# Optimization experiments

Measured on AMD Instinct MI355X. Metric: run time of the kernel, lower is better.

The kernel has to match this reference:

```python
import jax, jax.numpy as jnp
import numpy as np

B, C_IN, C_OUT = 2, 32, 32
N_IN = 128 * 128            # input grid points
N_OUT = 128 * 128           # output grid points
KERNEL_SIZE = 9             # (3-1)*4 + 1 for kernel_shape=[3,4], piecewise_linear basis
NNZ = 1_500_000             # sparse entries in psi (kernel_size, n_out, n_in)


def setup_inputs() -> dict:
    key = jax.random.key(0)
    ks = jax.random.split(key, 8)
    scale = (1.0 / C_IN) ** 0.5  # sqrt(1/groupsize), groups=1
    return {
        "x": jax.random.normal(ks[0], (B, C_IN, N_IN), jnp.float32),
        "quadrature_weights": jax.random.uniform(ks[1], (N_IN,), jnp.float32, 0.5, 1.5) / N_IN,
        "psi_vals": jax.random.uniform(ks[2], (NNZ,), jnp.float32),
        "weight": scale * jax.random.normal(ks[3], (C_OUT, C_IN, KERNEL_SIZE), jnp.float32),
        "bias": jnp.zeros((C_OUT,), jnp.float32),
        "psi_idx_k": jax.random.randint(ks[4], (NNZ,), 0, KERNEL_SIZE, dtype=jnp.int32),
        "psi_idx_out": jax.random.randint(ks[5], (NNZ,), 0, N_OUT, dtype=jnp.int32),
        "psi_idx_in": jax.random.randint(ks[6], (NNZ,), 0, N_IN, dtype=jnp.int32),
        "n_out": N_OUT,
    }


def reference(x, quadrature_weights, psi_vals, weight, bias,
              psi_idx_k, psi_idx_out, psi_idx_in, n_out):
    # x: (B, C, n_in); weight: (O, C, K); psi is sparse (K, n_out, n_in)
    Bb, C, n_in = x.shape
    K = weight.shape[2]
    # pre-multiply by quadrature weights, layout (n_in, B, C) for gather
    xq = (x * quadrature_weights[None, None, :]).transpose(2, 0, 1)
    # gather-weight: contribution of each sparse entry  -> (nnz, B, C)
    contrib = xq[psi_idx_in] * psi_vals[:, None, None]
    # scatter-add into (kernel, out) bins == sparse psi @ xq
    seg = psi_idx_k * n_out + psi_idx_out
    xk = jax.ops.segment_sum(contrib, seg, num_segments=K * n_out)
    xk = xk.reshape(K, n_out, Bb, C)  # (K, n_out, B, C)
    # channel/kernel mixing with learned weight (groups=1)
    out = jnp.einsum("knbc,ock->bon", xk, weight) + bias[None, :, None]
    return out  # (B, out_channels, n_out)
```

## Files before the change

kernel.cpp:

```cpp
#include <hip/hip_runtime.h>

#define N_IN   16384
#define N_OUT  16384
#define KSZ    9
#define CIN    32
#define COUT   32
#define BC     64
#define NCB    256
#define CHA    4096
#define ECAP_A 8192
#define ROWS   144
#define XSTR   68
#define SCAP   2048

union PrepSH {
    struct { int cnt[NCB]; int cntE[NCB]; int gbase[NCB]; int cursor[NCB];
             float2 slist[CHA]; } bin;
    struct { float tile[64 * 65]; } xqp;
};

__global__ __launch_bounds__(512) void k_prep(
        const float* __restrict__ x, const float* __restrict__ qw,
        const float* __restrict__ vals, const float* __restrict__ w,
        const int* __restrict__ ik, const int* __restrict__ io,
        const int* __restrict__ ii, float* __restrict__ xq,
        float2* __restrict__ sivA, int* __restrict__ gcntA,
        float* __restrict__ wT, int nnz, int nchA) {
    __shared__ PrepSH sh;
    const int t = threadIdx.x;
    const int bid = blockIdx.x;

    if (bid >= nchA) {
        if (bid < nchA + 256) {
            const int in0 = (bid - nchA) * 64;
#pragma unroll
            for (int i = 0; i < 8; ++i) {
                int idx = t + i * 512;
                int bcl = idx >> 6, inl = idx & 63;
                sh.xqp.tile[bcl * 65 + inl] = x[bcl * N_IN + in0 + inl];
            }
            __syncthreads();
#pragma unroll
            for (int i = 0; i < 8; ++i) {
                int idx = t + i * 512;
                int inl = idx >> 6, bcl = idx & 63;
                xq[(size_t)(in0 + inl) * BC + bcl] = sh.xqp.tile[bcl * 65 + inl] * qw[in0 + inl];
            }
        } else {
            for (int i = t; i < COUT * CIN * KSZ; i += 512) {
                int o = i / (CIN * KSZ);
                int r = i - o * (CIN * KSZ);
                int c = r / KSZ;
                int k = r - c * KSZ;
                wT[((k * 8 + (o >> 2)) * 32 + c) * 4 + (o & 3)] = w[i];
            }
        }
        return;
    }

    if (t < NCB) sh.bin.cnt[t] = 0;
    __syncthreads();
    const int base = bid * CHA;
    const int e0   = base + t * 8;

    float vv[8]; int pk[8]; int bk[8]; bool hv[8];
    if (e0 + 8 <= nnz) {
        int4 a0 = *(const int4*)(io + e0),  a1 = *(const int4*)(io + e0 + 4);
        int4 b0 = *(const int4*)(ii + e0),  b1 = *(const int4*)(ii + e0 + 4);
        int4 k0 = *(const int4*)(ik + e0),  k1 = *(const int4*)(ik + e0 + 4);
        float4 d0 = *(const float4*)(vals + e0), d1 = *(const float4*)(vals + e0 + 4);
        int ov[8] = {a0.x, a0.y, a0.z, a0.w, a1.x, a1.y, a1.z, a1.w};
        int iv[8] = {b0.x, b0.y, b0.z, b0.w, b1.x, b1.y, b1.z, b1.w};
        int kv[8] = {k0.x, k0.y, k0.z, k0.w, k1.x, k1.y, k1.z, k1.w};
        float dv[8] = {d0.x, d0.y, d0.z, d0.w, d1.x, d1.y, d1.z, d1.w};
#pragma unroll
        for (int j = 0; j < 8; ++j) {
            hv[j] = true;
            bk[j] = ov[j] >> 6;
            pk[j] = (int)(((unsigned)(ov[j] >> 4) << 22)) | (iv[j] << 8) | (kv[j] * 16 + (ov[j] & 15));
            vv[j] = dv[j];
        }
    } else {
#pragma unroll
        for (int j = 0; j < 8; ++j) {
            int e = e0 + j;
            hv[j] = (e < nnz);
            if (hv[j]) {
                int o = io[e];
                bk[j] = o >> 6;
                pk[j] = (int)(((unsigned)(o >> 4) << 22)) | (ii[e] << 8) | (ik[e] * 16 + (o & 15));
                vv[j] = vals[e];
            } else { bk[j] = 0; pk[j] = 0; vv[j] = 0.f; }
        }
    }
#pragma unroll
    for (int j = 0; j < 8; ++j) if (hv[j]) atomicAdd(&sh.bin.cnt[bk[j]], 1);
    __syncthreads();
    if (t < NCB) {
        int cv = sh.bin.cnt[t];
        sh.bin.gbase[t] = t * ECAP_A + (cv ? atomicAdd(&gcntA[t], cv) : 0);
    }
    if (t < 64) {
        int carry = 0;
#pragma unroll
        for (int seg = 0; seg < 4; ++seg) {
            int idx = seg * 64 + t;
            int v = sh.bin.cnt[idx];
            int orig = v;
#pragma unroll
            for (int off = 1; off < 64; off <<= 1) {
                int u = __shfl_up(v, off);
                if (t >= off) v += u;
            }
            sh.bin.cntE[idx]   = carry + v - orig;
            sh.bin.cursor[idx] = carry + v - orig;
            carry += __shfl(v, 63);
        }
    }
    __syncthreads();
#pragma unroll
    for (int j = 0; j < 8; ++j) {
        if (hv[j]) {
            int pos = atomicAdd(&sh.bin.cursor[bk[j]], 1);
            sh.bin.slist[pos] = make_float2(vv[j], __int_as_float(pk[j]));
        }
    }
    __syncthreads();
    const int m = min(nnz - base, CHA);
    for (int p = t; p < m; p += 512) {
        float2 f2 = sh.bin.slist[p];
        int cb = (int)((unsigned)__float_as_int(f2.y) >> 24);
        int dest = sh.bin.gbase[cb] + (p - sh.bin.cntE[cb]);
        if (dest < (cb + 1) * ECAP_A) sivA[dest] = f2;
    }
}

__global__ __launch_bounds__(512) void k_fused6(const float* __restrict__ xq,
        const float2* __restrict__ sivA, const int* __restrict__ gcntA,
        const float* __restrict__ wT, const float* __restrict__ bias,
        float* __restrict__ out) {
    __shared__ __align__(16) float sxk[80 * XSTR];
    __shared__ float2 slist[SCAP];
    __shared__ int    rowStart[ROWS + 1];
    __shared__ int    cursor[ROWS];
    __shared__ int    mcur;
    const int tid  = threadIdx.x;
    const int lane = tid & 63;
    const int wv   = __builtin_amdgcn_readfirstlane(tid >> 6);
    const unsigned f = ((blockIdx.x & 7) << 7) | (blockIdx.x >> 3);

    if (tid < ROWS) rowStart[tid] = 0;
    if (tid == 0) mcur = 0;
    __syncthreads();

    const int cb = (int)(f >> 2);
    const int mA = min(gcntA[cb], ECAP_A);
    const float2* src = sivA + (size_t)cb * ECAP_A;
    float2* tmp = (float2*)sxk;
    for (int i = tid; i < mA; i += 512) {
        float2 v = src[i];
        unsigned fid = (unsigned)__float_as_int(v.y) >> 22;
        if (fid == f) {
            int pos = atomicAdd(&mcur, 1);
            if (pos < SCAP) {
                tmp[pos] = v;
                atomicAdd(&rowStart[__float_as_int(v.y) & 0xFF], 1);
            }
        }
    }
    __syncthreads();
    const int m2 = min(mcur, SCAP);
    if (wv == 0) {
        int carry = 0;
#pragma unroll
        for (int i0 = 0; i0 < 192; i0 += 64) {
            int idx = i0 + lane;
            int v = (idx < ROWS) ? rowStart[idx] : 0;
            int orig = v;
#pragma unroll
            for (int off = 1; off < 64; off <<= 1) {
                int u = __shfl_up(v, off);
                if (lane >= off) v += u;
            }
            if (idx < ROWS) {
                int excl = carry + v - orig;
                rowStart[idx] = excl;
                cursor[idx]   = excl;
            }
            carry += __shfl(v, 63);
        }
        if (lane == 0) rowStart[ROWS] = carry;
    }
    __syncthreads();
    for (int i = tid; i < m2; i += 512) {
        float2 v = tmp[i];
        int p = __float_as_int(v.y);
        int pos = atomicAdd(&cursor[p & 0xFF], 1);
        slist[pos] = make_float2(v.x, __int_as_float(p & 0x3FFF00));
    }
    __syncthreads();

    const char* xqb   = (const char*)xq;
    const int   lane4 = lane * 4;
    const int   h     = lane >> 4;
    const int   nl    = lane & 15;
    float acc[4] = {0.f, 0.f, 0.f, 0.f};

#pragma unroll
    for (int ph = 0; ph < 2; ++ph) {
        const int rbase = ph ? 80 : 0;
        const int rend  = ph ? 144 : 80;
        const int nrows = rend - rbase;
        for (int i = tid; i < nrows * XSTR; i += 512) sxk[i] = 0.f;
        __syncthreads();
        for (int r = rbase + wv; r < rend; r += 8) {
            const int a = rowStart[r], b = rowStart[r + 1];
            if (a >= b) continue;
            float acc0 = 0.f, acc1 = 0.f, acc2 = 0.f, acc3 = 0.f;
            int i = a;
            for (; i + 7 < b; i += 8) {
                float2 v0 = slist[i],     v1 = slist[i + 1], v2 = slist[i + 2], v3 = slist[i + 3];
                float2 v4 = slist[i + 4], v5 = slist[i + 5], v6 = slist[i + 6], v7 = slist[i + 7];
                acc0 += *(const float*)(xqb + (__float_as_int(v0.y) + lane4)) * v0.x;
                acc1 += *(const float*)(xqb + (__float_as_int(v1.y) + lane4)) * v1.x;
                acc2 += *(const float*)(xqb + (__float_as_int(v2.y) + lane4)) * v2.x;
                acc3 += *(const float*)(xqb + (__float_as_int(v3.y) + lane4)) * v3.x;
                acc0 += *(const float*)(xqb + (__float_as_int(v4.y) + lane4)) * v4.x;
                acc1 += *(const float*)(xqb + (__float_as_int(v5.y) + lane4)) * v5.x;
                acc2 += *(const float*)(xqb + (__float_as_int(v6.y) + lane4)) * v6.x;
                acc3 += *(const float*)(xqb + (__float_as_int(v7.y) + lane4)) * v7.x;
            }
            for (; i + 3 < b; i += 4) {
                float2 v0 = slist[i], v1 = slist[i + 1], v2 = slist[i + 2], v3 = slist[i + 3];
                acc0 += *(const float*)(xqb + (__float_as_int(v0.y) + lane4)) * v0.x;
                acc1 += *(const float*)(xqb + (__float_as_int(v1.y) + lane4)) * v1.x;
                acc2 += *(const float*)(xqb + (__float_as_int(v2.y) + lane4)) * v2.x;
                acc3 += *(const float*)(xqb + (__float_as_int(v3.y) + lane4)) * v3.x;
            }
            for (; i < b; ++i) {
                float2 v = slist[i];
                acc0 += *(const float*)(xqb + (__float_as_int(v.y) + lane4)) * v.x;
            }
            sxk[(r - rbase) * XSTR + lane] = (acc0 + acc1) + (acc2 + acc3);
        }
        __syncthreads();
        if (lane < 32) {
            const int kbase = ph ? 5 : 0;
            const int kcnt  = ph ? 4 : 5;
            for (int kk = 0; kk < kcnt; ++kk) {
                const float* xr = &sxk[(kk * 16 + nl) * XSTR + h * 32];
                const float* wp = &wT[((kbase + kk) * 8 + wv) * 128];
#pragma unroll
                for (int c4 = 0; c4 < 8; ++c4) {
                    float4 xv = *(const float4*)&xr[c4 * 4];
#pragma unroll
                    for (int cc = 0; cc < 4; ++cc) {
                        float xval = (&xv.x)[cc];
#pragma unroll
                        for (int j = 0; j < 4; ++j)
                            acc[j] += xval * wp[(c4 * 4 + cc) * 4 + j];
                    }
                }
            }
        }
        __syncthreads();
    }

    if (lane < 32) {
        const int n0 = (int)f * 16;
#pragma unroll
        for (int j = 0; j < 4; ++j) {
            int o = wv * 4 + j;
            out[((size_t)h * COUT + o) * N_OUT + n0 + nl] = acc[j] + bias[o];
        }
    }
}

extern "C" void kernel_launch(void* const* d_in, const int* in_sizes, int n_in,
                              void* d_out, int out_size, void* d_ws, size_t ws_size,
                              hipStream_t stream) {
    const float* x    = (const float*)d_in[0];
    const float* qw   = (const float*)d_in[1];
    const float* vals = (const float*)d_in[2];
    const float* w    = (const float*)d_in[3];
    const float* bias = (const float*)d_in[4];
    const int*   ik   = (const int*)d_in[5];
    const int*   io   = (const int*)d_in[6];
    const int*   ii   = (const int*)d_in[7];
    const int    nnz  = in_sizes[2];
    const int    nchA = (nnz + CHA - 1) / CHA;

    char* ws = (char*)d_ws;
    float*  xq    = (float*)ws;  ws += (size_t)N_IN * BC * 4;
    float2* sivA  = (float2*)ws; ws += (size_t)NCB * ECAP_A * 8;
    int*    gcntA = (int*)ws;    ws += NCB * 4;
    float*  wT    = (float*)ws;  ws += (size_t)COUT * CIN * KSZ * 4;

    hipMemsetAsync(gcntA, 0, NCB * sizeof(int), stream);
    k_prep  <<<nchA + 257, 512, 0, stream>>>(x, qw, vals, w, ik, io, ii,
                                             xq, sivA, gcntA, wT, nnz, nchA);
    k_fused6<<<1024, 512, 0, stream>>>(xq, sivA, gcntA, wT, bias, (float*)d_out);
}
```

Before: 168.8 us.

## Merge prep and fused kernels into one cooperative persistent kernel with grid syncs

The memset, binning/prep kernel and fused gather-GEMM kernel become one cooperative kernel. Grid-wide syncs separate the counter reset, the binning phase and the compute phase, and blocks loop persistently over work items. Global bin counters are padded to a 16-int stride to avoid false sharing between atomics. This removes two launch gaps and the memset. In exchange the grid may be smaller than before (1024/512/256 blocks depending on queried occupancy), which adds grid-sync overhead and gives less parallelism if occupancy is low.

Measured after the change: 381.3 us. 126% more time.

```diff
diff --git a/kernel.cpp b/kernel.cpp
--- a/kernel.cpp
+++ b/kernel.cpp
@@ -1,4 +1,7 @@
 #include <hip/hip_runtime.h>
+#include <hip/hip_cooperative_groups.h>
+
+namespace cg = cooperative_groups;
 
 #define N_IN   16384
 #define N_OUT  16384
@@ -9,270 +12,275 @@
 #define NCB    256
 #define CHA    4096
 #define ECAP_A 8192
+#define GSTR   16
 #define ROWS   144
 #define XSTR   68
 #define SCAP   2048
-
-union PrepSH {
-    struct { int cnt[NCB]; int cntE[NCB]; int gbase[NCB]; int cursor[NCB];
-             float2 slist[CHA]; } bin;
-    struct { float tile[64 * 65]; } xqp;
-};
-
-__global__ __launch_bounds__(512) void k_prep(
+#define NSLICE 1024
+
+struct BinSH { int cnt[NCB]; int cntE[NCB]; int gbase[NCB]; int cursor[NCB];
+               float2 slist[CHA]; };
+struct XqSH  { float tile[64 * 65]; };
+struct FusSH { float sxk[80 * XSTR]; float2 slist[SCAP];
+               int rowStart[ROWS + 1]; int cursor[ROWS]; int mcur; };
+union __align__(16) MegaSH { BinSH bin; XqSH xqp; FusSH fus; };
+
+__global__ __launch_bounds__(512, 8) void k_mega(
         const float* __restrict__ x, const float* __restrict__ qw,
         const float* __restrict__ vals, const float* __restrict__ w,
+        const float* __restrict__ bias,
         const int* __restrict__ ik, const int* __restrict__ io,
         const int* __restrict__ ii, float* __restrict__ xq,
         float2* __restrict__ sivA, int* __restrict__ gcntA,
-        float* __restrict__ wT, int nnz, int nchA) {
-    __shared__ PrepSH sh;
-    const int t = threadIdx.x;
-    const int bid = blockIdx.x;
-
-    if (bid >= nchA) {
-        if (bid < nchA + 256) {
-            const int in0 = (bid - nchA) * 64;
-#pragma unroll
-            for (int i = 0; i < 8; ++i) {
-                int idx = t + i * 512;
-                int bcl = idx >> 6, inl = idx & 63;
-                sh.xqp.tile[bcl * 65 + inl] = x[bcl * N_IN + in0 + inl];
-            }
+        float* __restrict__ wT, float* __restrict__ out,
+        int nnz, int nchA) {
+    __shared__ MegaSH sh;
+    const int t    = threadIdx.x;
+    const int lane = t & 63;
+    const int wv   = __builtin_amdgcn_readfirstlane(t >> 6);
+
+    if (blockIdx.x == 0 && t < NCB) gcntA[t * GSTR] = 0;
+    cg::this_grid().sync();
+
+    for (int wk = blockIdx.x; wk < nchA + 257; wk += gridDim.x) {
+        if (wk >= nchA) {
+            if (wk < nchA + 256) {
+                const int in0 = (wk - nchA) * 64;
+#pragma unroll
+                for (int i = 0; i < 8; ++i) {
+                    int idx = t + i * 512;
+                    int bcl = idx >> 6, inl = idx & 63;
+                    sh.xqp.tile[bcl * 65 + inl] = x[bcl * N_IN + in0 + inl];
+                }
+                __syncthreads();
+#pragma unroll
+                for (int i = 0; i < 8; ++i) {
+                    int idx = t + i * 512;
+                    int inl = idx >> 6, bcl = idx & 63;
+                    xq[(size_t)(in0 + inl) * BC + bcl] = sh.xqp.tile[bcl * 65 + inl] * qw[in0 + inl];
+                }
+                __syncthreads();
+            } else {
+                for (int i = t; i < COUT * CIN * KSZ; i += 512) {
+                    int o = i / (CIN * KSZ);
+                    int r = i - o * (CIN * KSZ);
+                    int c = r / KSZ;
+                    int k = r - c * KSZ;
+                    wT[((k * 8 + (o >> 2)) * 32 + c) * 4 + (o & 3)] = w[i];
+                }
+            }
+            continue;
+        }
+        if (t < NCB) sh.bin.cnt[t] = 0;
+        __syncthreads();
+        const int base = wk * CHA;
+        const int e0   = base + t * 8;
+
+        float vv[8]; int pk[8]; int bk[8]; bool hv[8];
+        if (e0 + 8 <= nnz) {
+            int4 a0 = *(const int4*)(io + e0),  a1 = *(const int4*)(io + e0 + 4);
+            int4 b0 = *(const int4*)(ii + e0),  b1 = *(const int4*)(ii + e0 + 4);
+            int4 k0 = *(const int4*)(ik + e0),  k1 = *(const int4*)(ik + e0 + 4);
+            float4 d0 = *(const float4*)(vals + e0), d1 = *(const float4*)(vals + e0 + 4);
+            int ov[8] = {a0.x, a0.y, a0.z, a0.w, a1.x, a1.y, a1.z, a1.w};
+            int iv[8] = {b0.x, b0.y, b0.z, b0.w, b1.x, b1.y, b1.z, b1.w};
+            int kv[8] = {k0.x, k0.y, k0.z, k0.w, k1.x, k1.y, k1.z, k1.w};
+            float dv[8] = {d0.x, d0.y, d0.z, d0.w, d1.x, d1.y, d1.z, d1.w};
+#pragma unroll
+            for (int j = 0; j < 8; ++j) {
+                hv[j] = true;
+                bk[j] = ov[j] >> 6;
+                pk[j] = (int)(((unsigned)(ov[j] >> 4) << 22)) | (iv[j] << 8) | (kv[j] * 16 + (ov[j] & 15));
+                vv[j] = dv[j];
+            }
+        } else {
+#pragma unroll
+            for (int j = 0; j < 8; ++j) {
+                int e = e0 + j;
+                hv[j] = (e < nnz);
+                if (hv[j]) {
+                    int o = io[e];
+                    bk[j] = o >> 6;
+                    pk[j] = (int)(((unsigned)(o >> 4) << 22)) | (ii[e] << 8) | (ik[e] * 16 + (o & 15));
+                    vv[j] = vals[e];
+                } else { bk[j] = 0; pk[j] = 0; vv[j] = 0.f; }
+            }
+        }
+#pragma unroll
+        for (int j = 0; j < 8; ++j) if (hv[j]) atomicAdd(&sh.bin.cnt[bk[j]], 1);
+        __syncthreads();
+        if (t < NCB) {
+            int cv = sh.bin.cnt[t];
+            sh.bin.gbase[t] = t * ECAP_A + (cv ? atomicAdd(&gcntA[t * GSTR], cv) : 0);
+        }
+        if (t < 64) {
+            int carry = 0;
+#pragma unroll
+            for (int seg = 0; seg < 4; ++seg) {
+                int idx = seg * 64 + t;
+                int v = sh.bin.cnt[idx];
+                int orig = v;
+#pragma unroll
+                for (int off = 1; off < 64; off <<= 1) {
+                    int u = __shfl_up(v, off);
+                    if (t >= off) v += u;
+                }
+                sh.bin.cntE[idx]   = carry + v - orig;
+                sh.bin.cursor[idx] = carry + v - orig;
+                carry += __shfl(v, 63);
+            }
+        }
+        __syncthreads();
+#pragma unroll
+        for (int j = 0; j < 8; ++j) {
+            if (hv[j]) {
+                int pos = atomicAdd(&sh.bin.cursor[bk[j]], 1);
+                sh.bin.slist[pos] = make_float2(vv[j], __int_as_float(pk[j]));
+            }
+        }
+        __syncthreads();
+        const int m = min(nnz - base, CHA);
+        for (int p = t; p < m; p += 512) {
+            float2 f2 = sh.bin.slist[p];
+            int cb = (int)((unsigned)__float_as_int(f2.y) >> 24);
+            int dest = sh.bin.gbase[cb] + (p - sh.bin.cntE[cb]);
+            if (dest < (cb + 1) * ECAP_A) sivA[dest] = f2;
+        }
+        __syncthreads();
+    }
+
+    cg::this_grid().sync();
+
+    for (unsigned f = blockIdx.x; f < NSLICE; f += gridDim.x) {
+        if (t < ROWS) sh.fus.rowStart[t] = 0;
+        if (t == 0) sh.fus.mcur = 0;
+        __syncthreads();
+
+        const int cb = (int)(f >> 2);
+        const int mA = min(gcntA[cb * GSTR], ECAP_A);
+        const float2* src = sivA + (size_t)cb * ECAP_A;
+        float2* tmp = (float2*)sh.fus.sxk;
+        for (int i = t; i < mA; i += 512) {
+            float2 v = src[i];
+            unsigned fid = (unsigned)__float_as_int(v.y) >> 22;
+            if (fid == f) {
+                int pos = atomicAdd(&sh.fus.mcur, 1);
+                if (pos < SCAP) {
+                    tmp[pos] = v;
+                    atomicAdd(&sh.fus.rowStart[__float_as_int(v.y) & 0xFF], 1);
+                }
+            }
+        }
+        __syncthreads();
+        const int m2 = min(sh.fus.mcur, SCAP);
+        if (wv == 0) {
+            int carry = 0;
+#pragma unroll
+            for (int i0 = 0; i0 < 192; i0 += 64) {
+                int idx = i0 + lane;
+                int v = (idx < ROWS) ? sh.fus.rowStart[idx] : 0;
+                int orig = v;
+#pragma unroll
+                for (int off = 1; off < 64; off <<= 1) {
+                    int u = __shfl_up(v, off);
+                    if (lane >= off) v += u;
+                }
+                if (idx < ROWS) {
+                    int excl = carry + v - orig;
+                    sh.fus.rowStart[idx] = excl;
+                    sh.fus.cursor[idx]   = excl;
+                }
+                carry += __shfl(v, 63);
+            }
+            if (lane == 0) sh.fus.rowStart[ROWS] = carry;
+        }
+        __syncthreads();
+        for (int i = t; i < m2; i += 512) {
+            float2 v = tmp[i];
+            int p = __float_as_int(v.y);
+            int pos = atomicAdd(&sh.fus.cursor[p & 0xFF], 1);
+            sh.fus.slist[pos] = make_float2(v.x, __int_as_float(p & 0x3FFF00));
+        }
+        __syncthreads();
+
+        const char* xqb   = (const char*)xq;
+        const int   lane4 = lane * 4;
+        const int   h     = lane >> 4;
+        const int   nl    = lane & 15;
+        float acc[4] = {0.f, 0.f, 0.f, 0.f};
+
+#pragma unroll
+        for (int ph = 0; ph < 2; ++ph) {
+            const int rbase = ph ? 80 : 0;
+            const int rend  = ph ? 144 : 80;
+            const int nrows = rend - rbase;
+            for (int i = t; i < nrows * XSTR; i += 512) sh.fus.sxk[i] = 0.f;
             __syncthreads();
-#pragma unroll
-            for (int i = 0; i < 8; ++i) {
-                int idx = t + i * 512;
-                int inl = idx >> 6, bcl = idx & 63;
-                xq[(size_t)(in0 + inl) * BC + bcl] = sh.xqp.tile[bcl * 65 + inl] * qw[in0 + inl];
-            }
-        } else {
-            for (int i = t; i < COUT * CIN * KSZ; i += 512) {
-                int o = i / (CIN * KSZ);
-                int r = i - o * (CIN * KSZ);
-                int c = r / KSZ;
-                int k = r - c * KSZ;
-                wT[((k * 8 + (o >> 2)) * 32 + c) * 4 + (o & 3)] = w[i];
-            }
-        }
-        return;
-    }
-
-    if (t < NCB) sh.bin.cnt[t] = 0;
-    __syncthreads();
-    const int base = bid * CHA;
-    const int e0   = base + t * 8;
-
-    float vv[8]; int pk[8]; int bk[8]; bool hv[8];
-    if (e0 + 8 <= nnz) {
-        int4 a0 = *(const int4*)(io + e0),  a1 = *(const int4*)(io + e0 + 4);
-        int4 b0 = *(const int4*)(ii + e0),  b1 = *(const int4*)(ii + e0 + 4);
-        int4 k0 = *(const int4*)(ik + e0),  k1 = *(const int4*)(ik + e0 + 4);
-        float4 d0 = *(const float4*)(vals + e0), d1 = *(const float4*)(vals + e0 + 4);
-        int ov[8] = {a0.x, a0.y, a0.z, a0.w, a1.x, a1.y, a1.z, a1.w};
-        int iv[8] = {b0.x, b0.y, b0.z, b0.w, b1.x, b1.y, b1.z, b1.w};
-        int kv[8] = {k0.x, k0.y, k0.z, k0.w, k1.x, k1.y, k1.z, k1.w};
-        float dv[8] = {d0.x, d0.y, d0.z, d0.w, d1.x, d1.y, d1.z, d1.w};
-#pragma unroll
-        for (int j = 0; j < 8; ++j) {
-            hv[j] = true;
-            bk[j] = ov[j] >> 6;
-            pk[j] = (int)(((unsigned)(ov[j] >> 4) << 22)) | (iv[j] << 8) | (kv[j] * 16 + (ov[j] & 15));
-            vv[j] = dv[j];
-        }
-    } else {
-#pragma unroll
-        for (int j = 0; j < 8; ++j) {
-            int e = e0 + j;
-            hv[j] = (e < nnz);
-            if (hv[j]) {
-                int o = io[e];
-                bk[j] = o >> 6;
-                pk[j] = (int)(((unsigned)(o >> 4) << 22)) | (ii[e] << 8) | (ik[e] * 16 + (o & 15));
-                vv[j] = vals[e];
-            } else { bk[j] = 0; pk[j] = 0; vv[j] = 0.f; }
-        }
-    }
-#pragma unroll
-    for (int j = 0; j < 8; ++j) if (hv[j]) atomicAdd(&sh.bin.cnt[bk[j]], 1);
-    __syncthreads();
-    if (t < NCB) {
-        int cv = sh.bin.cnt[t];
-        sh.bin.gbase[t] = t * ECAP_A + (cv ? atomicAdd(&gcntA[t], cv) : 0);
-    }
-    if (t < 64) {
-        int carry = 0;
-#pragma unroll
-        for (int seg = 0; seg < 4; ++seg) {
-            int idx = seg * 64 + t;
-            int v = sh.bin.cnt[idx];
-            int orig = v;
-#pragma unroll
-            for (int off = 1; off < 64; off <<= 1) {
-                int u = __shfl_up(v, off);
-                if (t >= off) v += u;
-            }
-            sh.bin.cntE[idx]   = carry + v - orig;
-            sh.bin.cursor[idx] = carry + v - orig;
-            carry += __shfl(v, 63);
-        }
-    }
-    __syncthreads();
-#pragma unroll
-    for (int j = 0; j < 8; ++j) {
-        if (hv[j]) {
-            int pos = atomicAdd(&sh.bin.cursor[bk[j]], 1);
-            sh.bin.slist[pos] = make_float2(vv[j], __int_as_float(pk[j]));
-        }
-    }
-    __syncthreads();
-    const int m = min(nnz - base, CHA);
-    for (int p = t; p < m; p += 512) {
-        float2 f2 = sh.bin.slist[p];
-        int cb = (int)((unsigned)__float_as_int(f2.y) >> 24);
-        int dest = sh.bin.gbase[cb] + (p - sh.bin.cntE[cb]);
-        if (dest < (cb + 1) * ECAP_A) sivA[dest] = f2;
-    }
-}
-
-__global__ __launch_bounds__(512) void k_fused6(const float* __restrict__ xq,
-        const float2* __restrict__ sivA, const int* __restrict__ gcntA,
-        const float* __restrict__ wT, const float* __restrict__ bias,
-        float* __restrict__ out) {
-    __shared__ __align__(16) float sxk[80 * XSTR];
-    __shared__ float2 slist[SCAP];
-    __shared__ int    rowStart[ROWS + 1];
-    __shared__ int    cursor[ROWS];
-    __shared__ int    mcur;
-    const int tid  = threadIdx.x;
-    const int lane = tid & 63;
-    const int wv   = __builtin_amdgcn_readfirstlane(tid >> 6);
-    const unsigned f = ((blockIdx.x & 7) << 7) | (blockIdx.x >> 3);
-
-    if (tid < ROWS) rowStart[tid] = 0;
-    if (tid == 0) mcur = 0;
-    __syncthreads();
-
-    const int cb = (int)(f >> 2);
-    const int mA = min(gcntA[cb], ECAP_A);
-    const float2* src = sivA + (size_t)cb * ECAP_A;
-    float2* tmp = (float2*)sxk;
-    for (int i = tid; i < mA; i += 512) {
-        float2 v = src[i];
-        unsigned fid = (unsigned)__float_as_int(v.y) >> 22;
-        if (fid == f) {
-            int pos = atomicAdd(&mcur, 1);
-            if (pos < SCAP) {
-                tmp[pos] = v;
-                atomicAdd(&rowStart[__float_as_int(v.y) & 0xFF], 1);
-            }
-        }
-    }
-    __syncthreads();
-    const int m2 = min(mcur, SCAP);
-    if (wv == 0) {
-        int carry = 0;
-#pragma unroll
-        for (int i0 = 0; i0 < 192; i0 += 64) {
-            int idx = i0 + lane;
-            int v = (idx < ROWS) ? rowStart[idx] : 0;
-            int orig = v;
-#pragma unroll
-            for (int off = 1; off < 64; off <<= 1) {
-                int u = __shfl_up(v, off);
-                if (lane >= off) v += u;
-            }
-            if (idx < ROWS) {
-                int excl = carry + v - orig;
-                rowStart[idx] = excl;
-                cursor[idx]   = excl;
-            }
-            carry += __shfl(v, 63);
-        }
-        if (lane == 0) rowStart[ROWS] = carry;
-    }
-    __syncthreads();
-    for (int i = tid; i < m2; i += 512) {
-        float2 v = tmp[i];
-        int p = __float_as_int(v.y);
-        int pos = atomicAdd(&cursor[p & 0xFF], 1);
-        slist[pos] = make_float2(v.x, __int_as_float(p & 0x3FFF00));
-    }
-    __syncthreads();
-
-    const char* xqb   = (const char*)xq;
-    const int   lane4 = lane * 4;
-    const int   h     = lane >> 4;
-    const int   nl    = lane & 15;
-    float acc[4] = {0.f, 0.f, 0.f, 0.f};
-
-#pragma unroll
-    for (int ph = 0; ph < 2; ++ph) {
-        const int rbase = ph ? 80 : 0;
-        const int rend  = ph ? 144 : 80;
-        const int nrows = rend - rbase;
-        for (int i = tid; i < nrows * XSTR; i += 512) sxk[i] = 0.f;
-        __syncthreads();
-        for (int r = rbase + wv; r < rend; r += 8) {
-            const int a = rowStart[r], b = rowStart[r + 1];
-            if (a >= b) continue;
-            float acc0 = 0.f, acc1 = 0.f, acc2 = 0.f, acc3 = 0.f;
-            int i = a;
-            for (; i + 7 < b; i += 8) {
-                float2 v0 = slist[i],     v1 = slist[i + 1], v2 = slist[i + 2], v3 = slist[i + 3];
-                float2 v4 = slist[i + 4], v5 = slist[i + 5], v6 = slist[i + 6], v7 = slist[i + 7];
-                acc0 += *(const float*)(xqb + (__float_as_int(v0.y) + lane4)) * v0.x;
-                acc1 += *(const float*)(xqb + (__float_as_int(v1.y) + lane4)) * v1.x;
-                acc2 += *(const float*)(xqb + (__float_as_int(v2.y) + lane4)) * v2.x;
-                acc3 += *(const float*)(xqb + (__float_as_int(v3.y) + lane4)) * v3.x;
-                acc0 += *(const float*)(xqb + (__float_as_int(v4.y) + lane4)) * v4.x;
-                acc1 += *(const float*)(xqb + (__float_as_int(v5.y) + lane4)) * v5.x;
-                acc2 += *(const float*)(xqb + (__float_as_int(v6.y) + lane4)) * v6.x;
-                acc3 += *(const float*)(xqb + (__float_as_int(v7.y) + lane4)) * v7.x;
-            }
-            for (; i + 3 < b; i += 4) {
-                float2 v0 = slist[i], v1 = slist[i + 1], v2 = slist[i + 2], v3 = slist[i + 3];
-                acc0 += *(const float*)(xqb + (__float_as_int(v0.y) + lane4)) * v0.x;
-                acc1 += *(const float*)(xqb + (__float_as_int(v1.y) + lane4)) * v1.x;
-                acc2 += *(const float*)(xqb + (__float_as_int(v2.y) + lane4)) * v2.x;
-                acc3 += *(const float*)(xqb + (__float_as_int(v3.y) + lane4)) * v3.x;
-            }
-            for (; i < b; ++i) {
-                float2 v = slist[i];
-                acc0 += *(const float*)(xqb + (__float_as_int(v.y) + lane4)) * v.x;
-            }
-            sxk[(r - rbase) * XSTR + lane] = (acc0 + acc1) + (acc2 + acc3);
-        }
-        __syncthreads();
+            for (int r = rbase + wv; r < rend; r += 8) {
+                const int a = sh.fus.rowStart[r], b = sh.fus.rowStart[r + 1];
+                if (a >= b) continue;
+                float acc0 = 0.f, acc1 = 0.f, acc2 = 0.f, acc3 = 0.f;
+                int i = a;
+                for (; i + 7 < b; i += 8) {
+                    float2 v0 = sh.fus.slist[i],     v1 = sh.fus.slist[i + 1];
+                    float2 v2 = sh.fus.slist[i + 2], v3 = sh.fus.slist[i + 3];
+                    float2 v4 = sh.fus.slist[i + 4], v5 = sh.fus.slist[i + 5];
+                    float2 v6 = sh.fus.slist[i + 6], v7 = sh.fus.slist[i + 7];
+                    acc0 += *(const float*)(xqb + (__float_as_int(v0.y) + lane4)) * v0.x;
+                    acc1 += *(const float*)(xqb + (__float_as_int(v1.y) + lane4)) * v1.x;
+                    acc2 += *(const float*)(xqb + (__float_as_int(v2.y) + lane4)) * v2.x;
+                    acc3 += *(const float*)(xqb + (__float_as_int(v3.y) + lane4)) * v3.x;
+                    acc0 += *(const float*)(xqb + (__float_as_int(v4.y) + lane4)) * v4.x;
+                    acc1 += *(const float*)(xqb + (__float_as_int(v5.y) + lane4)) * v5.x;
+                    acc2 += *(const float*)(xqb + (__float_as_int(v6.y) + lane4)) * v6.x;
+                    acc3 += *(const float*)(xqb + (__float_as_int(v7.y) + lane4)) * v7.x;
+                }
+                for (; i + 3 < b; i += 4) {
+                    float2 v0 = sh.fus.slist[i],     v1 = sh.fus.slist[i + 1];
+                    float2 v2 = sh.fus.slist[i + 2], v3 = sh.fus.slist[i + 3];
+                    acc0 += *(const float*)(xqb + (__float_as_int(v0.y) + lane4)) * v0.x;
+                    acc1 += *(const float*)(xqb + (__float_as_int(v1.y) + lane4)) * v1.x;
+                    acc2 += *(const float*)(xqb + (__float_as_int(v2.y) + lane4)) * v2.x;
+                    acc3 += *(const float*)(xqb + (__float_as_int(v3.y) + lane4)) * v3.x;
+                }
+                for (; i < b; ++i) {
+                    float2 v = sh.fus.slist[i];
+                    acc0 += *(const float*)(xqb + (__float_as_int(v.y) + lane4)) * v.x;
+                }
+                sh.fus.sxk[(r - rbase) * XSTR + lane] = (acc0 + acc1) + (acc2 + acc3);
+            }
+            __syncthreads();
+            if (lane < 32) {
+                const int kbase = ph ? 5 : 0;
+                const int kcnt  = ph ? 4 : 5;
+                for (int kk = 0; kk < kcnt; ++kk) {
+                    const float* xr = &sh.fus.sxk[(kk * 16 + nl) * XSTR + h * 32];
+                    const float* wp = &wT[((kbase + kk) * 8 + wv) * 128];
+#pragma unroll
+                    for (int c4 = 0; c4 < 8; ++c4) {
+                        float4 xv = *(const float4*)&xr[c4 * 4];
+#pragma unroll
+                        for (int cc = 0; cc < 4; ++cc) {
+                            float xval = (&xv.x)[cc];
+#pragma unroll
+                            for (int j = 0; j < 4; ++j)
+                                acc[j] += xval * wp[(c4 * 4 + cc) * 4 + j];
+                        }
+                    }
+                }
+            }
+            __syncthreads();
+        }
+
         if (lane < 32) {
-            const int kbase = ph ? 5 : 0;
-            const int kcnt  = ph ? 4 : 5;
-            for (int kk = 0; kk < kcnt; ++kk) {
-                const float* xr = &sxk[(kk * 16 + nl) * XSTR + h * 32];
-                const float* wp = &wT[((kbase + kk) * 8 + wv) * 128];
-#pragma unroll
-                for (int c4 = 0; c4 < 8; ++c4) {
-                    float4 xv = *(const float4*)&xr[c4 * 4];
-#pragma unroll
-                    for (int cc = 0; cc < 4; ++cc) {
-                        float xval = (&xv.x)[cc];
-#pragma unroll
-                        for (int j = 0; j < 4; ++j)
-                            acc[j] += xval * wp[(c4 * 4 + cc) * 4 + j];
-                    }
-                }
-            }
-        }
-        __syncthreads();
-    }
-
-    if (lane < 32) {
-        const int n0 = (int)f * 16;
-#pragma unroll
-        for (int j = 0; j < 4; ++j) {
-            int o = wv * 4 + j;
-            out[((size_t)h * COUT + o) * N_OUT + n0 + nl] = acc[j] + bias[o];
-        }
+            const int n0 = (int)f * 16;
+#pragma unroll
+            for (int j = 0; j < 4; ++j) {
+                int o = wv * 4 + j;
+                out[((size_t)h * COUT + o) * N_OUT + n0 + nl] = acc[j] + bias[o];
+            }
+        }
+        __syncthreads();
     }
 }
 
@@ -287,17 +295,28 @@
     const int*   ik   = (const int*)d_in[5];
     const int*   io   = (const int*)d_in[6];
     const int*   ii   = (const int*)d_in[7];
-    const int    nnz  = in_sizes[2];
-    const int    nchA = (nnz + CHA - 1) / CHA;
+    int          nnz  = in_sizes[2];
+    int          nchA = (nnz + CHA - 1) / CHA;
 
     char* ws = (char*)d_ws;
     float*  xq    = (float*)ws;  ws += (size_t)N_IN * BC * 4;
     float2* sivA  = (float2*)ws; ws += (size_t)NCB * ECAP_A * 8;
-    int*    gcntA = (int*)ws;    ws += NCB * 4;
+    int*    gcntA = (int*)ws;    ws += (size_t)NCB * GSTR * 4;
     float*  wT    = (float*)ws;  ws += (size_t)COUT * CIN * KSZ * 4;
-
-    hipMemsetAsync(gcntA, 0, NCB * sizeof(int), stream);
-    k_prep  <<<nchA + 257, 512, 0, stream>>>(x, qw, vals, w, ik, io, ii,
-                                             xq, sivA, gcntA, wT, nnz, nchA);
-    k_fused6<<<1024, 512, 0, stream>>>(xq, sivA, gcntA, wT, bias, (float*)d_out);
+    float*  out   = (float*)d_out;
+
+    static int nblk = 0;
+    if (nblk == 0) {
+        int occ = 0;
+        if (hipOccupancyMaxActiveBlocksPerMultiprocessor(&occ, (const void*)k_mega,
+                                                         512, 0) != hipSuccess || occ < 1)
+            occ = 1;
+        nblk = (occ >= 4) ? 1024 : (occ >= 2 ? 512 : 256);
+    }
+
+    void* args[] = { (void*)&x, (void*)&qw, (void*)&vals, (void*)&w, (void*)&bias,
+                     (void*)&ik, (void*)&io, (void*)&ii, (void*)&xq, (void*)&sivA,
+                     (void*)&gcntA, (void*)&wT, (void*)&out, (void*)&nnz, (void*)&nchA };
+    hipLaunchCooperativeKernel((const void*)k_mega, dim3(nblk), dim3(512),
+                               args, 0, stream);
 }
```
